# Kernel optimization log

Hardware: AMD Instinct MI355X
Metric: run time of the kernel (lower is better)

The kernel has to match this reference:

```python
import jax, jax.numpy as jnp
import numpy as np

N = 2048
EMBED_DIM = 64
N_SUBJ, N_REL, N_OBJ = 16, 9, 16


def setup_inputs() -> dict:
    key = jax.random.key(0)
    ks = jax.random.split(key, 16)
    scale = 0.05  # keep sigmoid unsaturated
    return {
        "subj_idx": jax.random.randint(ks[0], (N,), 0, N_SUBJ, dtype=jnp.int32),
        "rel_idx": jax.random.randint(ks[1], (N,), 0, N_REL, dtype=jnp.int32),
        "obj_idx": jax.random.randint(ks[2], (N,), 0, N_OBJ, dtype=jnp.int32),
        "subj_table": jax.random.normal(ks[3], (N_SUBJ, EMBED_DIM), jnp.float32),
        "rel_table": jax.random.normal(ks[4], (N_REL, EMBED_DIM), jnp.float32),
        "obj_table": jax.random.normal(ks[5], (N_OBJ, EMBED_DIM), jnp.float32),
        "proj_w": jax.random.normal(ks[6], (EMBED_DIM, 3 * EMBED_DIM), jnp.float32) * scale,
        "proj_b": jax.random.normal(ks[7], (EMBED_DIM,), jnp.float32) * scale,
        "w1": jax.random.normal(ks[8], (EMBED_DIM, 2 * EMBED_DIM), jnp.float32) * scale,
        "b1": jax.random.normal(ks[9], (EMBED_DIM,), jnp.float32) * scale,
        "w2": jax.random.normal(ks[10], (32, EMBED_DIM), jnp.float32) * scale,
        "b2": jax.random.normal(ks[11], (32,), jnp.float32) * scale,
        "w3": jax.random.normal(ks[12], (1, 32), jnp.float32) * scale,
        "b3": jax.random.normal(ks[13], (1,), jnp.float32) * scale,
    }


def reference(subj_idx, rel_idx, obj_idx, subj_table, rel_table, obj_table,
              proj_w, proj_b, w1, b1, w2, b2, w3, b3):
    # --- ClaimEmbedder.embed, batched over all N claims ---
    # combined [N, 3*D] = cat(subj, rel, obj) embeddings; proj -> [N, D]
    combined = jnp.concatenate(
        [subj_table[subj_idx], rel_table[rel_idx], obj_table[obj_idx]], axis=-1)
    e = combined @ proj_w.T + proj_b  # [N, D]

    # --- conflict_scorer over all ordered pairs (i, j) ---
    # Linear(2D -> D) on cat(e_i, e_j) == e_i @ W1a.T + e_j @ W1b.T + b1
    d = e.shape[-1]
    w1a, w1b = w1[:, :d], w1[:, d:]
    hi = e @ w1a.T          # [N, D] contribution of left claim
    hj = e @ w1b.T          # [N, D] contribution of right claim
    h = jax.nn.relu(hi[:, None, :] + hj[None, :, :] + b1)  # [N, N, D]
    # Dropout(0.1) is identity in eval / no_grad inference.
    h2 = jax.nn.relu(jnp.einsum('ijd,kd->ijk', h, w2) + b2)  # [N, N, 32]
    scores = jax.nn.sigmoid(jnp.einsum('ijk,k->ij', h2, w3[0]) + b3[0])  # [N, N]
    # Only pairs with i < j are scored in the original nested loop.
    return jnp.triu(scores, k=1)
```

## Files before the change

kernel.cpp:

```cpp
#include <hip/hip_runtime.h>
#include <hip/hip_bf16.h>

#define NROWS 2048
#define HH 72

typedef __attribute__((ext_vector_type(4))) float f32x4;
typedef _Float16 f16x2 __attribute__((ext_vector_type(2)));
typedef _Float16 f16x8 __attribute__((ext_vector_type(8)));
typedef __fp16 fp16x2_raw __attribute__((ext_vector_type(2)));

union H8 { f16x8 v; f16x2 h2[4]; };

static __device__ __forceinline__ f32x4 vmax0(f32x4 a) {
    return __builtin_elementwise_max(a, (f32x4)0.f);
}
static __device__ __forceinline__ f16x8 hmax0(f16x8 a) {
    return __builtin_elementwise_max(a, (f16x8)(_Float16)0.f);
}
static __device__ __forceinline__ f16x2 pkrtz(float a, float b) {
    union { fp16x2_raw r; f16x2 f; } c;
    c.r = __builtin_amdgcn_cvt_pkrtz(a, b);
    return c.f;
}

#define TJ_OFF  2688
#define ET_OFF  5376

__global__ __launch_bounds__(256) void etab_kernel(
    const float* __restrict__ subj_table, const float* __restrict__ rel_table,
    const float* __restrict__ obj_table,
    const float* __restrict__ proj_w, const float* __restrict__ proj_b,
    float* __restrict__ ws)
{
    float* ET = ws + ET_OFF;
    const int r = blockIdx.x;
    const int lane = threadIdx.x & 63;
    const int w = threadIdx.x >> 6;

    if (r == 41) {
        if (threadIdx.x < 64) ET[41 * 64 + threadIdx.x] = proj_b[threadIdx.x];
        return;
    }
    const float* src; int off;
    if (r < 16)      { src = subj_table + r * 64;        off = 0;   }
    else if (r < 25) { src = rel_table + (r - 16) * 64;  off = 64;  }
    else             { src = obj_table + (r - 25) * 64;  off = 128; }
    const float sv = src[lane];

    #pragma unroll
    for (int t = 0; t < 4; ++t) {
        const int d0 = w * 16 + t * 4;
        float p0 = sv * proj_w[(d0 + 0) * 192 + off + lane];
        float p1 = sv * proj_w[(d0 + 1) * 192 + off + lane];
        float p2 = sv * proj_w[(d0 + 2) * 192 + off + lane];
        float p3 = sv * proj_w[(d0 + 3) * 192 + off + lane];
        #pragma unroll
        for (int m = 1; m < 64; m <<= 1) {
            p0 += __shfl_xor(p0, m, 64);
            p1 += __shfl_xor(p1, m, 64);
            p2 += __shfl_xor(p2, m, 64);
            p3 += __shfl_xor(p3, m, 64);
        }
        if (lane == 0) {
            ET[r * 64 + d0 + 0] = p0;
            ET[r * 64 + d0 + 1] = p1;
            ET[r * 64 + d0 + 2] = p2;
            ET[r * 64 + d0 + 3] = p3;
        }
    }
}

__global__ __launch_bounds__(256) void htab_kernel(
    const float* __restrict__ w1, const float* __restrict__ b1,
    float* __restrict__ ws)
{
    const float* ET = ws + ET_OFF;
    const int b = blockIdx.x;
    const int side = b & 1;
    const int r = b >> 1;
    const int lane = threadIdx.x & 63;
    const int w = threadIdx.x >> 6;

    float* dst = ws + (side ? TJ_OFF : 0);
    const float sv = ET[r * 64 + lane];
    const int woff = side * 64;

    #pragma unroll
    for (int t = 0; t < 4; ++t) {
        const int d0 = w * 16 + t * 4;
        float p0 = sv * w1[(d0 + 0) * 128 + woff + lane];
        float p1 = sv * w1[(d0 + 1) * 128 + woff + lane];
        float p2 = sv * w1[(d0 + 2) * 128 + woff + lane];
        float p3 = sv * w1[(d0 + 3) * 128 + woff + lane];
        #pragma unroll
        for (int m = 1; m < 64; m <<= 1) {
            p0 += __shfl_xor(p0, m, 64);
            p1 += __shfl_xor(p1, m, 64);
            p2 += __shfl_xor(p2, m, 64);
            p3 += __shfl_xor(p3, m, 64);
        }
        if (lane == 0) {
            const bool cst = (side == 0) && (r == 41);
            dst[r * 64 + d0 + 0] = p0 + (cst ? b1[d0 + 0] : 0.f);
            dst[r * 64 + d0 + 1] = p1 + (cst ? b1[d0 + 1] : 0.f);
            dst[r * 64 + d0 + 2] = p2 + (cst ? b1[d0 + 2] : 0.f);
            dst[r * 64 + d0 + 3] = p3 + (cst ? b1[d0 + 3] : 0.f);
        }
    }
}

__global__ __launch_bounds__(256, 4) void pair_kernel(
    const int* __restrict__ subj_idx, const int* __restrict__ rel_idx,
    const int* __restrict__ obj_idx,
    const float* __restrict__ tab,
    const float* __restrict__ w2, const float* __restrict__ b2,
    const float* __restrict__ w3, const float* __restrict__ b3,
    float* __restrict__ out)
{
    const int bx = blockIdx.x, by = blockIdx.y;
    const int i0 = by * 32, j0 = bx * 32;
    const int tid = threadIdx.x;

    if (bx < by) {
        const float4 z = {0.f, 0.f, 0.f, 0.f};
        ((float4*)(out + (size_t)(i0 + (tid >> 3)) * NROWS + j0))[tid & 7] = z;
        return;
    }

    __shared__ _Float16 hiL[32 * HH];
    __shared__ _Float16 hjL[32 * HH];

    const int lane = tid & 63;
    const int wid  = tid >> 6;
    const int col  = lane & 15;
    const int quad = lane >> 4;
    const int wj   = wid & 1;
    const int wi   = wid >> 1;

    {
        const int rr = tid >> 3;
        const int cc = (tid & 7) * 8;
        const int iR = i0 + rr, jR = j0 + rr;
        const int si = subj_idx[iR], ri = 16 + rel_idx[iR], oi = 25 + obj_idx[iR];
        const int sj = subj_idx[jR], rj = 16 + rel_idx[jR], oj = 25 + obj_idx[jR];
        const float* TI = tab;
        const float* TJ = tab + TJ_OFF;
        const f32x4 v0 = *(const f32x4*)(TI + si * 64 + cc)
                       + *(const f32x4*)(TI + ri * 64 + cc)
                       + *(const f32x4*)(TI + oi * 64 + cc)
                       + *(const f32x4*)(TI + 41 * 64 + cc);
        const f32x4 v1 = *(const f32x4*)(TI + si * 64 + cc + 4)
                       + *(const f32x4*)(TI + ri * 64 + cc + 4)
                       + *(const f32x4*)(TI + oi * 64 + cc + 4)
                       + *(const f32x4*)(TI + 41 * 64 + cc + 4);
        H8 hp;
        hp.h2[0] = pkrtz(v0[0], v0[1]); hp.h2[1] = pkrtz(v0[2], v0[3]);
        hp.h2[2] = pkrtz(v1[0], v1[1]); hp.h2[3] = pkrtz(v1[2], v1[3]);
        *(f16x8*)&hiL[rr * HH + cc] = hp.v;

        const f32x4 u0 = *(const f32x4*)(TJ + sj * 64 + cc)
                       + *(const f32x4*)(TJ + rj * 64 + cc)
                       + *(const f32x4*)(TJ + oj * 64 + cc)
                       + *(const f32x4*)(TJ + 41 * 64 + cc);
        const f32x4 u1 = *(const f32x4*)(TJ + sj * 64 + cc + 4)
                       + *(const f32x4*)(TJ + rj * 64 + cc + 4)
                       + *(const f32x4*)(TJ + oj * 64 + cc + 4)
                       + *(const f32x4*)(TJ + 41 * 64 + cc + 4);
        H8 hq;
        hq.h2[0] = pkrtz(u0[0], u0[1]); hq.h2[1] = pkrtz(u0[2], u0[3]);
        hq.h2[2] = pkrtz(u1[0], u1[1]); hq.h2[3] = pkrtz(u1[2], u1[3]);
        *(f16x8*)&hjL[rr * HH + cc] = hq.v;
    }

    H8 wf[2][2];
    #pragma unroll
    for (int ch = 0; ch < 2; ++ch)
        #pragma unroll
        for (int ks = 0; ks < 2; ++ks) {
            const f32x4* wr = (const f32x4*)(w2 + (ch * 16 + col) * 64 + ks * 32 + quad * 8);
            const f32x4 w0 = wr[0], w1v = wr[1];
            wf[ch][ks].h2[0] = pkrtz(w0[0], w0[1]);
            wf[ch][ks].h2[1] = pkrtz(w0[2], w0[3]);
            wf[ch][ks].h2[2] = pkrtz(w1v[0], w1v[1]);
            wf[ch][ks].h2[3] = pkrtz(w1v[2], w1v[3]);
        }
    const f32x4 b2A = *(const f32x4*)(b2 + quad * 4);
    const f32x4 b2B = *(const f32x4*)(b2 + 16 + quad * 4);
    const f32x4 w3A = *(const f32x4*)(w3 + quad * 4);
    const f32x4 w3B = *(const f32x4*)(w3 + 16 + quad * 4);
    const float b3v = b3[0];

    __syncthreads();

    const int hjb = (wj * 16 + col) * HH + quad * 8;
    const f16x8 hj0 = *(const f16x8*)&hjL[hjb];
    const f16x8 hj1 = *(const f16x8*)&hjL[hjb + 32];

    const int jg = j0 + wj * 16 + col;

    #pragma unroll 4
    for (int it = 0; it < 16; ++it) {
        const int il = wi * 16 + it;
        const int base = il * HH + quad * 8;
        const f16x8 x0 = *(const f16x8*)&hiL[base];
        const f16x8 x1 = *(const f16x8*)&hiL[base + 32];

        const f16x8 f0 = hmax0(x0 + hj0);
        const f16x8 f1 = hmax0(x1 + hj1);

        f32x4 accA = b2A;
        f32x4 accB = b2B;
        accA = __builtin_amdgcn_mfma_f32_16x16x32_f16(wf[0][0].v, f0, accA, 0, 0, 0);
        accA = __builtin_amdgcn_mfma_f32_16x16x32_f16(wf[0][1].v, f1, accA, 0, 0, 0);
        accB = __builtin_amdgcn_mfma_f32_16x16x32_f16(wf[1][0].v, f0, accB, 0, 0, 0);
        accB = __builtin_amdgcn_mfma_f32_16x16x32_f16(wf[1][1].v, f1, accB, 0, 0, 0);

        const f32x4 ra = vmax0(accA);
        const f32x4 rb = vmax0(accB);
        const f32x4 t4 = ra * w3A + rb * w3B;
        float p = (t4[0] + t4[1]) + (t4[2] + t4[3]);
        p += __shfl_xor(p, 16, 64);
        p += __shfl_xor(p, 32, 64);

        if (quad == 0) {
            const int i = i0 + il;
            const float score = 1.f / (1.f + __expf(-(p + b3v)));
            out[(size_t)i * NROWS + jg] = (jg > i) ? score : 0.f;
        }
    }
}

extern "C" void kernel_launch(void* const* d_in, const int* in_sizes, int n_in,
                              void* d_out, int out_size, void* d_ws, size_t ws_size,
                              hipStream_t stream) {
    const int*   subj_idx   = (const int*)d_in[0];
    const int*   rel_idx    = (const int*)d_in[1];
    const int*   obj_idx    = (const int*)d_in[2];
    const float* subj_table = (const float*)d_in[3];
    const float* rel_table  = (const float*)d_in[4];
    const float* obj_table  = (const float*)d_in[5];
    const float* proj_w     = (const float*)d_in[6];
    const float* proj_b     = (const float*)d_in[7];
    const float* w1         = (const float*)d_in[8];
    const float* b1         = (const float*)d_in[9];
    const float* w2         = (const float*)d_in[10];
    const float* b2         = (const float*)d_in[11];
    const float* w3         = (const float*)d_in[12];
    const float* b3         = (const float*)d_in[13];
    float* out = (float*)d_out;
    float* ws  = (float*)d_ws;

    etab_kernel<<<dim3(42), dim3(256), 0, stream>>>(
        subj_table, rel_table, obj_table, proj_w, proj_b, ws);

    htab_kernel<<<dim3(84), dim3(256), 0, stream>>>(w1, b1, ws);

    pair_kernel<<<dim3(NROWS / 32, NROWS / 32), dim3(256), 0, stream>>>(
        subj_idx, rel_idx, obj_idx, ws, w2, b2, w3, b3, out);
}
```

Before: 120.1 us.

## Fuse table kernels and batch pair-score reduction through shared memory with vector stores

Merges the two small precompute kernels into one launch. Each block recomputes its projected embedding row into shared memory, which removes a launch and the global round trip for the intermediate table. In the pair kernel, the per-iteration cross-quad shuffle reduction and the scalar store from one quarter of the lanes are replaced. Each wave instead writes its partial sums to a padded shared buffer and then does one pass that sums them, applies the sigmoid and mask, and writes float4 stores. This costs extra shared memory per block, which may reduce occupancy, and adds a second pass over the partials.

```diff
diff --git a/kernel.cpp b/kernel.cpp
--- a/kernel.cpp
+++ b/kernel.cpp
@@ -24,36 +24,62 @@
 }
 
 #define TJ_OFF  2688
-#define ET_OFF  5376
-
-__global__ __launch_bounds__(256) void etab_kernel(
+
+__global__ __launch_bounds__(256) void tab_kernel(
     const float* __restrict__ subj_table, const float* __restrict__ rel_table,
     const float* __restrict__ obj_table,
     const float* __restrict__ proj_w, const float* __restrict__ proj_b,
+    const float* __restrict__ w1, const float* __restrict__ b1,
     float* __restrict__ ws)
 {
-    float* ET = ws + ET_OFF;
-    const int r = blockIdx.x;
-    const int lane = threadIdx.x & 63;
-    const int w = threadIdx.x >> 6;
+    __shared__ float et[64];
+    const int b = blockIdx.x;
+    const int side = b & 1;
+    const int r = b >> 1;
+    const int tid = threadIdx.x;
+    const int lane = tid & 63;
+    const int w = tid >> 6;
 
     if (r == 41) {
-        if (threadIdx.x < 64) ET[41 * 64 + threadIdx.x] = proj_b[threadIdx.x];
-        return;
-    }
-    const float* src; int off;
-    if (r < 16)      { src = subj_table + r * 64;        off = 0;   }
-    else if (r < 25) { src = rel_table + (r - 16) * 64;  off = 64;  }
-    else             { src = obj_table + (r - 25) * 64;  off = 128; }
-    const float sv = src[lane];
-
+        if (tid < 64) et[tid] = proj_b[tid];
+    } else {
+        const float* src; int off;
+        if (r < 16)      { src = subj_table + r * 64;        off = 0;   }
+        else if (r < 25) { src = rel_table + (r - 16) * 64;  off = 64;  }
+        else             { src = obj_table + (r - 25) * 64;  off = 128; }
+        const float sv = src[lane];
+        #pragma unroll
+        for (int t = 0; t < 4; ++t) {
+            const int d0 = w * 16 + t * 4;
+            float p0 = sv * proj_w[(d0 + 0) * 192 + off + lane];
+            float p1 = sv * proj_w[(d0 + 1) * 192 + off + lane];
+            float p2 = sv * proj_w[(d0 + 2) * 192 + off + lane];
+            float p3 = sv * proj_w[(d0 + 3) * 192 + off + lane];
+            #pragma unroll
+            for (int m = 1; m < 64; m <<= 1) {
+                p0 += __shfl_xor(p0, m, 64);
+                p1 += __shfl_xor(p1, m, 64);
+                p2 += __shfl_xor(p2, m, 64);
+                p3 += __shfl_xor(p3, m, 64);
+            }
+            if (lane == 0) {
+                et[d0 + 0] = p0; et[d0 + 1] = p1;
+                et[d0 + 2] = p2; et[d0 + 3] = p3;
+            }
+        }
+    }
+    __syncthreads();
+
+    float* dst = ws + (side ? TJ_OFF : 0);
+    const float sv2 = et[lane];
+    const int woff = side * 64;
     #pragma unroll
     for (int t = 0; t < 4; ++t) {
         const int d0 = w * 16 + t * 4;
-        float p0 = sv * proj_w[(d0 + 0) * 192 + off + lane];
-        float p1 = sv * proj_w[(d0 + 1) * 192 + off + lane];
-        float p2 = sv * proj_w[(d0 + 2) * 192 + off + lane];
-        float p3 = sv * proj_w[(d0 + 3) * 192 + off + lane];
+        float p0 = sv2 * w1[(d0 + 0) * 128 + woff + lane];
+        float p1 = sv2 * w1[(d0 + 1) * 128 + woff + lane];
+        float p2 = sv2 * w1[(d0 + 2) * 128 + woff + lane];
+        float p3 = sv2 * w1[(d0 + 3) * 128 + woff + lane];
         #pragma unroll
         for (int m = 1; m < 64; m <<= 1) {
             p0 += __shfl_xor(p0, m, 64);
@@ -62,44 +88,6 @@
             p3 += __shfl_xor(p3, m, 64);
         }
         if (lane == 0) {
-            ET[r * 64 + d0 + 0] = p0;
-            ET[r * 64 + d0 + 1] = p1;
-            ET[r * 64 + d0 + 2] = p2;
-            ET[r * 64 + d0 + 3] = p3;
-        }
-    }
-}
-
-__global__ __launch_bounds__(256) void htab_kernel(
-    const float* __restrict__ w1, const float* __restrict__ b1,
-    float* __restrict__ ws)
-{
-    const float* ET = ws + ET_OFF;
-    const int b = blockIdx.x;
-    const int side = b & 1;
-    const int r = b >> 1;
-    const int lane = threadIdx.x & 63;
-    const int w = threadIdx.x >> 6;
-
-    float* dst = ws + (side ? TJ_OFF : 0);
-    const float sv = ET[r * 64 + lane];
-    const int woff = side * 64;
-
-    #pragma unroll
-    for (int t = 0; t < 4; ++t) {
-        const int d0 = w * 16 + t * 4;
-        float p0 = sv * w1[(d0 + 0) * 128 + woff + lane];
-        float p1 = sv * w1[(d0 + 1) * 128 + woff + lane];
-        float p2 = sv * w1[(d0 + 2) * 128 + woff + lane];
-        float p3 = sv * w1[(d0 + 3) * 128 + woff + lane];
-        #pragma unroll
-        for (int m = 1; m < 64; m <<= 1) {
-            p0 += __shfl_xor(p0, m, 64);
-            p1 += __shfl_xor(p1, m, 64);
-            p2 += __shfl_xor(p2, m, 64);
-            p3 += __shfl_xor(p3, m, 64);
-        }
-        if (lane == 0) {
             const bool cst = (side == 0) && (r == 41);
             dst[r * 64 + d0 + 0] = p0 + (cst ? b1[d0 + 0] : 0.f);
             dst[r * 64 + d0 + 1] = p1 + (cst ? b1[d0 + 1] : 0.f);
@@ -108,6 +96,8 @@
         }
     }
 }
+
+#define PSTR 68
 
 __global__ __launch_bounds__(256, 4) void pair_kernel(
     const int* __restrict__ subj_idx, const int* __restrict__ rel_idx,
@@ -129,6 +119,7 @@
 
     __shared__ _Float16 hiL[32 * HH];
     __shared__ _Float16 hjL[32 * HH];
+    __shared__ float part[4 * 16 * PSTR];
 
     const int lane = tid & 63;
     const int wid  = tid >> 6;
@@ -196,12 +187,11 @@
     const f16x8 hj0 = *(const f16x8*)&hjL[hjb];
     const f16x8 hj1 = *(const f16x8*)&hjL[hjb + 32];
 
-    const int jg = j0 + wj * 16 + col;
-
-    #pragma unroll 4
+    float* mypart = &part[wid * 16 * PSTR];
+
+    #pragma unroll 8
     for (int it = 0; it < 16; ++it) {
-        const int il = wi * 16 + it;
-        const int base = il * HH + quad * 8;
+        const int base = (wi * 16 + it) * HH + quad * 8;
         const f16x8 x0 = *(const f16x8*)&hiL[base];
         const f16x8 x1 = *(const f16x8*)&hiL[base + 32];
 
@@ -218,15 +208,25 @@
         const f32x4 ra = vmax0(accA);
         const f32x4 rb = vmax0(accB);
         const f32x4 t4 = ra * w3A + rb * w3B;
-        float p = (t4[0] + t4[1]) + (t4[2] + t4[3]);
-        p += __shfl_xor(p, 16, 64);
-        p += __shfl_xor(p, 32, 64);
-
-        if (quad == 0) {
-            const int i = i0 + il;
-            const float score = 1.f / (1.f + __expf(-(p + b3v)));
-            out[(size_t)i * NROWS + jg] = (jg > i) ? score : 0.f;
-        }
+        mypart[it * PSTR + quad * 16 + col] = (t4[0] + t4[1]) + (t4[2] + t4[3]);
+    }
+
+    {
+        const int sub = lane & 3;
+        const int itx = lane >> 2;
+        const float* pr = &mypart[itx * PSTR + sub * 4];
+        const f32x4 s = *(const f32x4*)(pr)
+                      + *(const f32x4*)(pr + 16)
+                      + *(const f32x4*)(pr + 32)
+                      + *(const f32x4*)(pr + 48);
+        const int i  = i0 + wi * 16 + itx;
+        const int jb = j0 + wj * 16 + sub * 4;
+        float4 o;
+        o.x = (jb + 0 > i) ? 1.f / (1.f + __expf(-(s[0] + b3v))) : 0.f;
+        o.y = (jb + 1 > i) ? 1.f / (1.f + __expf(-(s[1] + b3v))) : 0.f;
+        o.z = (jb + 2 > i) ? 1.f / (1.f + __expf(-(s[2] + b3v))) : 0.f;
+        o.w = (jb + 3 > i) ? 1.f / (1.f + __expf(-(s[3] + b3v))) : 0.f;
+        *(float4*)(out + (size_t)i * NROWS + jb) = o;
     }
 }
 
@@ -250,10 +250,8 @@
     float* out = (float*)d_out;
     float* ws  = (float*)d_ws;
 
-    etab_kernel<<<dim3(42), dim3(256), 0, stream>>>(
-        subj_table, rel_table, obj_table, proj_w, proj_b, ws);
-
-    htab_kernel<<<dim3(84), dim3(256), 0, stream>>>(w1, b1, ws);
+    tab_kernel<<<dim3(84), dim3(256), 0, stream>>>(
+        subj_table, rel_table, obj_table, proj_w, proj_b, w1, b1, ws);
 
     pair_kernel<<<dim3(NROWS / 32, NROWS / 32), dim3(256), 0, stream>>>(
         subj_idx, rel_idx, obj_idx, ws, w2, b2, w3, b3, out);
```

Result: faster. 115.9 us (-3.5%).
